# Performance work log

Measured on AMD Instinct MI355X. Metric: run time of the kernel, lower is better.

The kernel has to match this reference:

```python
import jax, jax.numpy as jnp
import numpy as np

B_LAYERS = 4      # no_of_base_layers
A = 2048          # no_of_aux_layers
E_LAYERS = 4      # no_of_end_layers
H = 256           # nodes_in_each_layer
IN = 1            # input_shape
OUT = 2           # output_shape
NUM_LAYERS = B_LAYERS + A + E_LAYERS + 1


def setup_inputs() -> dict:
    key = jax.random.key(0)
    ks = jax.random.split(key, 24)
    s = 0.02
    f32 = jnp.float32
    d = {}
    d["X"] = jax.random.normal(ks[0], (A,), f32)
    d["X_mask"] = jax.random.randint(ks[1], (A,), 0, 2) > 0
    d["base_feature"] = jax.random.normal(ks[2], (IN,), f32)
    # base stack: Linear(IN,H)+ReLU then (B_LAYERS-1) x Linear(H,H)+ReLU; per-layer out heads Linear(H,OUT)+Softmax
    d["Wb_first"] = jax.random.normal(ks[3], (IN, H), f32) * s
    d["bb_first"] = jnp.zeros((H,), f32)
    d["Wb_rest"] = jax.random.normal(ks[4], (B_LAYERS - 1, H, H), f32) * s
    d["bb_rest"] = jnp.zeros((B_LAYERS - 1, H), f32)
    d["Wbo"] = jax.random.normal(ks[5], (B_LAYERS, H, OUT), f32) * s
    d["bbo"] = jnp.zeros((B_LAYERS, OUT), f32)
    # middle layer
    d["Wm"] = jax.random.normal(ks[6], (H, H), f32) * s
    d["bm"] = jnp.zeros((H,), f32)
    d["Wmo"] = jax.random.normal(ks[7], (H, OUT), f32) * s
    d["bmo"] = jnp.zeros((OUT,), f32)
    # aux experts: A x (Linear(1,H)+ReLU) and A x (Linear(H,OUT)+Softmax)
    d["Wa"] = jax.random.normal(ks[8], (A, H), f32) * s
    d["ba"] = jnp.zeros((A, H), f32)
    d["Wao"] = jax.random.normal(ks[9], (A, H, OUT), f32) * s
    d["bao"] = jnp.zeros((A, OUT), f32)
    # end stack: Linear((A+1)*H, H) then (E_LAYERS-1) x Linear(H,H); per-layer heads
    d["We_first"] = jax.random.normal(ks[10], ((A + 1) * H, H), f32) * s
    d["be_first"] = jnp.zeros((H,), f32)
    d["We_rest"] = jax.random.normal(ks[11], (E_LAYERS - 1, H, H), f32) * s
    d["be_rest"] = jnp.zeros((E_LAYERS - 1, H), f32)
    d["Weo"] = jax.random.normal(ks[12], (E_LAYERS, H, OUT), f32) * s
    d["beo"] = jnp.zeros((E_LAYERS, OUT), f32)
    d["layer_weights"] = jnp.full((NUM_LAYERS,), 1.0 / NUM_LAYERS, f32)
    return d


def reference(X, X_mask, base_feature, Wb_first, bb_first, Wb_rest, bb_rest,
              Wbo, bbo, Wm, bm, Wmo, bmo, Wa, ba, Wao, bao,
              We_first, be_first, We_rest, be_rest, Weo, beo, layer_weights):
    dt = X.dtype
    # --- base stack ---
    x = base_feature.reshape(1, -1)
    x = jax.nn.relu(x @ Wb_first + bb_first)
    outs = [jax.nn.softmax(x @ Wbo[0] + bbo[0], axis=-1)]
    for i in range(B_LAYERS - 1):
        x = jax.nn.relu(x @ Wb_rest[i] + bb_rest[i])
        outs.append(jax.nn.softmax(x @ Wbo[i + 1] + bbo[i + 1], axis=-1))
    # --- middle ---
    middle = jax.nn.relu(x @ Wm + bm)                       # [1, H]
    middle_out = jax.nn.softmax(middle @ Wmo + bmo, axis=-1)
    # --- aux experts, vectorized over all A features (absent ones are masked out) ---
    h = jax.nn.relu(X[:, None] * Wa + ba)                   # [A, H]
    aux_out = jax.nn.softmax(jnp.einsum('ah,aho->ao', h, Wao) + bao, axis=-1)  # [A, OUT]
    mask = X_mask.astype(dt)                                # [A]
    # --- weighted scatter-combine into end_input ---
    end_input = jnp.concatenate([h * mask[:, None], middle], axis=0)  # [A+1, H]
    gamma = jnp.concatenate([layer_weights[B_LAYERS:B_LAYERS + A], layer_weights[-1:]])
    gmask = jnp.concatenate([mask, jnp.ones((1,), dt)])
    gamma = gamma * gmask
    gamma = gamma / jnp.sum(gamma)
    x = (end_input * gamma[:, None]).reshape(1, -1)         # [1, (A+1)*H]
    # --- end stack ---
    end_outs = []
    x = jax.nn.relu(x @ We_first + be_first)
    end_outs.append(jax.nn.softmax(x @ Weo[0] + beo[0], axis=-1))
    for i in range(E_LAYERS - 1):
        x = jax.nn.relu(x @ We_rest[i] + be_rest[i])
        end_outs.append(jax.nn.softmax(x @ Weo[i + 1] + beo[i + 1], axis=-1))
    # --- hedge-weighted combine (order: base, aux, end, middle == layer_weights order) ---
    logits = jnp.concatenate(outs + [aux_out] + end_outs + [middle_out], axis=0)  # [NUM_LAYERS, OUT]
    active = jnp.concatenate([jnp.ones((B_LAYERS,), dt), mask, jnp.ones((E_LAYERS + 1,), dt)])
    w = layer_weights * active
    w = w / jnp.sum(w)
    logits_w = logits * w[:, None]
    logit = jnp.sum(logits_w, axis=0)
    return (logit, logits_w)
```

## Files before the change

### kernel.cpp

```cpp
#include <hip/hip_runtime.h>
#include <math.h>

#define A_N 2048
#define NLAYERS 2057

#define PART_OFF  0
#define PART2_OFF 524544
#define GSUM_OFF  540928
#define WSUM_OFF  540929
#define NACTI_OFF 540930
#define LISTI_OFF 540932

typedef float f4 __attribute__((ext_vector_type(4)));

__device__ __forceinline__ void warmN(const float* base, int nf4, int t, int nthr)
{
    const f4* p = (const f4*)base;
    for (int i = t; i < nf4; i += nthr) {
        f4 v = p[i];
        asm volatile("" :: "v"(v.x), "v"(v.y), "v"(v.z), "v"(v.w));
    }
}


__device__ __forceinline__ void head256(const float* sx, float* r0, float* r1,
                                        const float* W2, const float* b2,
                                        float scale, float* dest, int t)
{
    float xv = sx[t];
    r0[t] = xv * W2[2*t];
    r1[t] = xv * W2[2*t+1];
    __syncthreads();
    for (int s = 128; s > 0; s >>= 1) {
        if (t < s) { r0[t] += r0[t+s]; r1[t] += r1[t+s]; }
        __syncthreads();
    }
    if (t == 0) {
        float o0 = r0[0] + b2[0], o1 = r1[0] + b2[1];
        float m  = fmaxf(o0, o1);
        float e0 = expf(o0 - m), e1 = expf(o1 - m);
        float inv = scale / (e0 + e1);
        dest[0] = e0 * inv;
        dest[1] = e1 * inv;
    }
    __syncthreads();
}

__device__ __forceinline__ int compact_nz(float val, int t, int quad, int lane,
                                          int* rlist, float* gl, int* swcnt)
{
    bool pred = (val != 0.f);
    unsigned long long m = __ballot(pred);
    if (lane == 0) swcnt[quad] = (int)__popcll(m);
    __syncthreads();
    int nr = swcnt[0] + swcnt[1] + swcnt[2] + swcnt[3];
    int offs = 0;
    #pragma unroll
    for (int q2 = 0; q2 < 4; ++q2) if (q2 < quad) offs += swcnt[q2];
    int rank = (int)__popcll(m & ((1ull << lane) - 1ull));
    if (pred) { rlist[offs + rank] = t; gl[offs + rank] = val; }
    if (t < 32) { rlist[nr + t] = 0; gl[nr + t] = 0.f; }
    __syncthreads();
    return nr;
}

__device__ __forceinline__ f4 gather8(const f4* Wb, const int* rlist,
                                      const float* gl, int nr, int quad)
{
    f4 acc = {0.f, 0.f, 0.f, 0.f};
    int niter = (nr + 31) >> 5;
    for (int it = 0; it < niter; ++it) {
        int base = it*32 + quad*8;
        int r0 = rlist[base+0], r1 = rlist[base+1], r2 = rlist[base+2], r3 = rlist[base+3];
        int r4 = rlist[base+4], r5 = rlist[base+5], r6 = rlist[base+6], r7 = rlist[base+7];
        float g0 = gl[base+0], g1 = gl[base+1], g2 = gl[base+2], g3 = gl[base+3];
        float g4 = gl[base+4], g5 = gl[base+5], g6 = gl[base+6], g7 = gl[base+7];
        f4 v0 = Wb[(size_t)r0*64]; f4 v1 = Wb[(size_t)r1*64];
        f4 v2 = Wb[(size_t)r2*64]; f4 v3 = Wb[(size_t)r3*64];
        f4 v4 = Wb[(size_t)r4*64]; f4 v5 = Wb[(size_t)r5*64];
        f4 v6 = Wb[(size_t)r6*64]; f4 v7 = Wb[(size_t)r7*64];
        acc += g0*v0 + g1*v1 + g2*v2 + g3*v3 + g4*v4 + g5*v5 + g6*v6 + g7*v7;
    }
    return acc;
}

__global__ __launch_bounds__(1024) void k_list(const int* __restrict__ Xm,
                                               const float* __restrict__ lw,
                                               const float* __restrict__ Wbr,
                                               const float* __restrict__ Wm,
                                               const float* __restrict__ Wbo,
                                               const float* __restrict__ Wmo,
                                               const float* __restrict__ Wef,
                                               float* __restrict__ out,
                                               float* __restrict__ ws)
{
    int t = threadIdx.x, b = blockIdx.x;
    if (b > 0) {
        int wi = b - 1;
        if      (wi < 12) warmN(Wbr + (size_t)wi * 16384, 4096, t, 1024);
        else if (wi < 16) warmN(Wm + (size_t)(wi - 12) * 16384, 4096, t, 1024);
        else if (wi == 16) { warmN(Wbo, 512, t, 1024); warmN(Wmo, 128, t, 1024); }
        else warmN(Wef + (size_t)A_N * 65536 + (size_t)(wi - 17) * 16384, 4096, t, 1024);
        return;
    }
    __shared__ int scan[1024];
    __shared__ float fred[1024];
    int e0 = 2*t, e1 = 2*t + 1;
    int a0 = (Xm[e0] != 0) ? 1 : 0;
    int a1 = (Xm[e1] != 0) ? 1 : 0;
    int s = a0 + a1;
    scan[t] = s;
    fred[t] = (a0 ? lw[4+e0] : 0.f) + (a1 ? lw[4+e1] : 0.f);
    __syncthreads();
    for (int off = 1; off < 1024; off <<= 1) {
        int v = (t >= off) ? scan[t-off] : 0;
        __syncthreads();
        scan[t] += v;
        __syncthreads();
    }
    for (int ss = 512; ss > 0; ss >>= 1) {
        if (t < ss) fred[t] += fred[t+ss];
        __syncthreads();
    }
    int total = scan[1023];
    int excl  = scan[t] - s;
    int* list = (int*)ws + LISTI_OFF;
    if (a0) list[excl] = e0;
    else    { out[2 + (4+e0)*2] = 0.f; out[2 + (4+e0)*2 + 1] = 0.f; }
    if (a1) list[excl + a0] = e1;
    else    { out[2 + (4+e1)*2] = 0.f; out[2 + (4+e1)*2 + 1] = 0.f; }
    if (t == 0) {
        ((int*)ws)[NACTI_OFF] = total;
        float gaux = fred[0];
        ws[GSUM_OFF] = gaux + lw[2056];
        ws[WSUM_OFF] = lw[0]+lw[1]+lw[2]+lw[3] + gaux
                     + lw[2052]+lw[2053]+lw[2054]+lw[2055]+lw[2056];
    }
}

__global__ __launch_bounds__(256, 4) void k_mainc(
    const float* __restrict__ X,
    const float* __restrict__ bfv,
    const float* __restrict__ Wbf, const float* __restrict__ bbf,
    const float* __restrict__ Wbr, const float* __restrict__ bbr,
    const float* __restrict__ Wbo, const float* __restrict__ bbo,
    const float* __restrict__ Wm, const float* __restrict__ bm,
    const float* __restrict__ Wmo, const float* __restrict__ bmo,
    const float* __restrict__ Wa, const float* __restrict__ ba,
    const float* __restrict__ Wao, const float* __restrict__ bao,
    const float* __restrict__ Wef, const float* __restrict__ lw,
    float* __restrict__ out, float* __restrict__ ws)
{
    __shared__ float sg[256];
    __shared__ float sacc[4][256];
    __shared__ float gl[288];
    __shared__ int   rlist[288];
    __shared__ int   swcnt[4];
    int b = blockIdx.x, t = threadIdx.x;
    int quad = t >> 6, lane = t & 63;
    float* part = ws + PART_OFF;

    if (b == 0) {
        sg[t] = fmaxf(bfv[0] * Wbf[t] + bbf[t], 0.f);
        __syncthreads();
        head256(sg, sacc[0], sacc[1], Wbo, bbo, lw[0], out + 2, t);

        #define MV_GATED(W, B)                                                  \
        {                                                                       \
            int nr = compact_nz(sg[t], t, quad, lane, rlist, gl, swcnt);        \
            f4 a = gather8((const f4*)(W) + lane, rlist, gl, nr, quad);         \
            sacc[quad][lane*4+0] = a.x; sacc[quad][lane*4+1] = a.y;             \
            sacc[quad][lane*4+2] = a.z; sacc[quad][lane*4+3] = a.w;             \
            __syncthreads();                                                    \
            float v = fmaxf(sacc[0][t] + sacc[1][t] + sacc[2][t] + sacc[3][t]   \
                            + (B)[t], 0.f);                                     \
            __syncthreads();                                                    \
            sg[t] = v;                                                          \
            __syncthreads();                                                    \
        }

        for (int i = 0; i < 3; ++i) {
            MV_GATED(Wbr + i*65536, bbr + i*256);
            head256(sg, sacc[0], sacc[1], Wbo + (i+1)*512, bbo + (i+1)*2,
                    lw[i+1], out + 2 + (i+1)*2, t);
        }
        MV_GATED(Wm, bm);
        head256(sg, sacc[0], sacc[1], Wmo, bmo, lw[2056], out + 2 + 2056*2, t);

        {
            int nr = compact_nz(sg[t] * lw[2056], t, quad, lane, rlist, gl, swcnt);
            f4 a = gather8((const f4*)(Wef + (size_t)A_N * 65536) + lane,
                           rlist, gl, nr, quad);
            sacc[quad][lane*4+0] = a.x; sacc[quad][lane*4+1] = a.y;
            sacc[quad][lane*4+2] = a.z; sacc[quad][lane*4+3] = a.w;
            __syncthreads();
            part[t] = sacc[0][t] + sacc[1][t] + sacc[2][t] + sacc[3][t];
        }
        return;
    }

    int idx = b - 1;
    int nact = ((const int*)ws)[NACTI_OFF];
    if (idx >= nact) return;
    int e = ((const int*)ws + LISTI_OFF)[idx];

    float xv = X[e];
    float w  = lw[4 + e];
    float h  = fmaxf(xv * Wa[e*256 + t] + ba[e*256 + t], 0.f);
    float2 wo = *(const float2*)&Wao[(size_t)e*512 + 2*t];
    sacc[0][t] = h * wo.x;
    sacc[1][t] = h * wo.y;
    __syncthreads();
    for (int s = 128; s > 0; s >>= 1) {
        if (t < s) { sacc[0][t] += sacc[0][t+s]; sacc[1][t] += sacc[1][t+s]; }
        __syncthreads();
    }
    if (t == 0) {
        float o0 = sacc[0][0] + bao[2*e], o1 = sacc[1][0] + bao[2*e+1];
        float m  = fmaxf(o0, o1);
        float e0 = expf(o0 - m), e1 = expf(o1 - m);
        float inv = w / (e0 + e1);
        out[2 + (4+e)*2]     = e0 * inv;
        out[2 + (4+e)*2 + 1] = e1 * inv;
    }
    float val = h * w;
    __syncthreads();

    int nr = compact_nz(val, t, quad, lane, rlist, gl, swcnt);
    f4 acc = gather8((const f4*)(Wef + (size_t)e * 65536) + lane, rlist, gl, nr, quad);
    sacc[quad][lane*4+0] = acc.x; sacc[quad][lane*4+1] = acc.y;
    sacc[quad][lane*4+2] = acc.z; sacc[quad][lane*4+3] = acc.w;
    __syncthreads();
    part[(size_t)(1+idx)*256 + t] = sacc[0][t] + sacc[1][t] + sacc[2][t] + sacc[3][t];
}

__global__ __launch_bounds__(256) void k_red(
    const float* __restrict__ Wer, const float* __restrict__ Weo,
    const float* __restrict__ bef, const float* __restrict__ ber,
    const float* __restrict__ beo, float* __restrict__ ws)
{
    int r = blockIdx.x, t = threadIdx.x;
    if (r < 48) warmN(Wer + (size_t)r * 4096, 1024, t, 256);
    else if (r == 48) {
        warmN(Weo, 512, t, 256); warmN(bef, 64, t, 256);
        warmN(ber, 192, t, 256); warmN(beo, 2, t, 256);
    }
    int nact = ((const int*)ws)[NACTI_OFF];
    float acc = 0.f;
    for (int j = r; j <= nact; j += 64) {
        acc += ws[PART_OFF + (size_t)j*256 + t];
    }
    ws[PART2_OFF + r*256 + t] = acc;
}

__global__ __launch_bounds__(1024) void k_end(
    const float* __restrict__ bef, const float* __restrict__ Wer,
    const float* __restrict__ ber, const float* __restrict__ Weo,
    const float* __restrict__ beo, const float* __restrict__ lw,
    float* __restrict__ out, float* __restrict__ ws)
{
    __shared__ float sx[256];
    __shared__ float racc[4][256];
    __shared__ float red0[1024], red1[1024];
    __shared__ float endraw[4][2];
    int tid = threadIdx.x;
    int q = tid >> 8, t = tid & 255;

    float acc = 0.f;
    #pragma unroll
    for (int j = 0; j < 16; ++j) acc += ws[PART2_OFF + (q*16 + j)*256 + t];
    racc[q][t] = acc;
    __syncthreads();
    float gsum = ws[GSUM_OFF];
    if (tid < 256) {
        float v = racc[0][t] + racc[1][t] + racc[2][t] + racc[3][t];
        sx[t] = fmaxf(v / gsum + bef[t], 0.f);
    }
    __syncthreads();

    #define HEAD_G(W2, B2, SCALE, DEST)                                         \
    {                                                                           \
        if (tid < 256) { red0[tid] = sx[tid]*(W2)[2*tid]; red1[tid] = sx[tid]*(W2)[2*tid+1]; } \
        __syncthreads();                                                        \
        for (int s = 128; s > 0; s >>= 1) {                                     \
            if (tid < s) { red0[tid] += red0[tid+s]; red1[tid] += red1[tid+s]; }\
            __syncthreads();                                                    \
        }                                                                       \
        if (tid == 0) {                                                         \
            float o0 = red0[0] + (B2)[0], o1 = red1[0] + (B2)[1];               \
            float m  = fmaxf(o0, o1);                                           \
            float e0 = expf(o0 - m), e1 = expf(o1 - m);                         \
            float inv = (SCALE) / (e0 + e1);                                    \
            (DEST)[0] = e0 * inv; (DEST)[1] = e1 * inv;                         \
        }                                                                       \
        __syncthreads();                                                        \
    }

    HEAD_G(Weo, beo, lw[2052], &endraw[0][0]);
    for (int i = 0; i < 3; ++i) {
        const float* Wq = Wer + i*65536 + (q*64)*256;
        float a2 = 0.f;
        #pragma unroll 16
        for (int k = 0; k < 64; ++k) a2 += sx[q*64 + k] * Wq[k*256 + t];
        racc[q][t] = a2;
        __syncthreads();
        if (tid < 256) {
            float v = racc[0][t] + racc[1][t] + racc[2][t] + racc[3][t];
            sx[t] = fmaxf(v + ber[i*256 + t], 0.f);
        }
        __syncthreads();
        HEAD_G(Weo + (i+1)*512, beo + (i+1)*2, lw[2053 + i], &endraw[i+1][0]);
    }

    float invw = 1.f / ws[WSUM_OFF];
    float s0 = 0.f, s1 = 0.f;
    for (int i = tid; i < NLAYERS; i += 1024) {
        float v0, v1;
        if (i >= 2052 && i < 2056) { v0 = endraw[i-2052][0]; v1 = endraw[i-2052][1]; }
        else                        { v0 = out[2 + 2*i];      v1 = out[2 + 2*i + 1]; }
        v0 *= invw; v1 *= invw;
        out[2 + 2*i]     = v0;
        out[2 + 2*i + 1] = v1;
        s0 += v0; s1 += v1;
    }
    red0[tid] = s0; red1[tid] = s1; __syncthreads();
    for (int s = 512; s > 0; s >>= 1) {
        if (tid < s) { red0[tid] += red0[tid+s]; red1[tid] += red1[tid+s]; }
        __syncthreads();
    }
    if (tid == 0) { out[0] = red0[0]; out[1] = red1[0]; }
}

extern "C" void kernel_launch(void* const* d_in, const int* in_sizes, int n_in,
                              void* d_out, int out_size, void* d_ws, size_t ws_size,
                              hipStream_t stream)
{
    const float* X    = (const float*)d_in[0];
    const int*   Xm   = (const int*)  d_in[1];
    const float* bfv  = (const float*)d_in[2];
    const float* Wbf  = (const float*)d_in[3];
    const float* bbf  = (const float*)d_in[4];
    const float* Wbr  = (const float*)d_in[5];
    const float* bbr  = (const float*)d_in[6];
    const float* Wbo  = (const float*)d_in[7];
    const float* bbo  = (const float*)d_in[8];
    const float* Wm   = (const float*)d_in[9];
    const float* bm   = (const float*)d_in[10];
    const float* Wmo  = (const float*)d_in[11];
    const float* bmo  = (const float*)d_in[12];
    const float* Wa   = (const float*)d_in[13];
    const float* ba   = (const float*)d_in[14];
    const float* Wao  = (const float*)d_in[15];
    const float* bao  = (const float*)d_in[16];
    const float* Wef  = (const float*)d_in[17];
    const float* bef  = (const float*)d_in[18];
    const float* Wer  = (const float*)d_in[19];
    const float* ber  = (const float*)d_in[20];
    const float* Weo  = (const float*)d_in[21];
    const float* beo  = (const float*)d_in[22];
    const float* lw   = (const float*)d_in[23];
    float* out = (float*)d_out;
    float* wsf = (float*)d_ws;

    k_list<<<22, 1024, 0, stream>>>(Xm, lw, Wbr, Wm, Wbo, Wmo, Wef, out, wsf);
    k_mainc<<<A_N + 1, 256, 0, stream>>>(X, bfv, Wbf, bbf, Wbr, bbr, Wbo, bbo,
                                         Wm, bm, Wmo, bmo, Wa, ba, Wao, bao,
                                         Wef, lw, out, wsf);
    k_red<<<64, 256, 0, stream>>>(Wer, Weo, bef, ber, beo, wsf);
    k_end<<<1, 1024, 0, stream>>>(bef, Wer, ber, Weo, beo, lw, out, wsf);
}
```

Baseline: 66.03 us.

## Drop the compaction kernel and gate aux blocks directly on the mask

Removes the k_list prefix-scan kernel, so each aux block now reads the mask and exits early when its expert is inactive. The cache-warming moves into the first blocks of the main kernel, and the gamma and weight sums are recomputed inside the final kernel. The end-stack matvec is also restructured to use 16 wavefronts with float4 loads. This saves one kernel launch and its serial scan, but k_red now walks all 2048 slots with a mask check, and the warming blocks delay aux expert work.

```diff
diff --git a/kernel.cpp b/kernel.cpp
--- a/kernel.cpp
+++ b/kernel.cpp
@@ -6,10 +6,6 @@
 
 #define PART_OFF  0
 #define PART2_OFF 524544
-#define GSUM_OFF  540928
-#define WSUM_OFF  540929
-#define NACTI_OFF 540930
-#define LISTI_OFF 540932
 
 typedef float f4 __attribute__((ext_vector_type(4)));
 
@@ -84,62 +80,8 @@
     return acc;
 }
 
-__global__ __launch_bounds__(1024) void k_list(const int* __restrict__ Xm,
-                                               const float* __restrict__ lw,
-                                               const float* __restrict__ Wbr,
-                                               const float* __restrict__ Wm,
-                                               const float* __restrict__ Wbo,
-                                               const float* __restrict__ Wmo,
-                                               const float* __restrict__ Wef,
-                                               float* __restrict__ out,
-                                               float* __restrict__ ws)
-{
-    int t = threadIdx.x, b = blockIdx.x;
-    if (b > 0) {
-        int wi = b - 1;
-        if      (wi < 12) warmN(Wbr + (size_t)wi * 16384, 4096, t, 1024);
-        else if (wi < 16) warmN(Wm + (size_t)(wi - 12) * 16384, 4096, t, 1024);
-        else if (wi == 16) { warmN(Wbo, 512, t, 1024); warmN(Wmo, 128, t, 1024); }
-        else warmN(Wef + (size_t)A_N * 65536 + (size_t)(wi - 17) * 16384, 4096, t, 1024);
-        return;
-    }
-    __shared__ int scan[1024];
-    __shared__ float fred[1024];
-    int e0 = 2*t, e1 = 2*t + 1;
-    int a0 = (Xm[e0] != 0) ? 1 : 0;
-    int a1 = (Xm[e1] != 0) ? 1 : 0;
-    int s = a0 + a1;
-    scan[t] = s;
-    fred[t] = (a0 ? lw[4+e0] : 0.f) + (a1 ? lw[4+e1] : 0.f);
-    __syncthreads();
-    for (int off = 1; off < 1024; off <<= 1) {
-        int v = (t >= off) ? scan[t-off] : 0;
-        __syncthreads();
-        scan[t] += v;
-        __syncthreads();
-    }
-    for (int ss = 512; ss > 0; ss >>= 1) {
-        if (t < ss) fred[t] += fred[t+ss];
-        __syncthreads();
-    }
-    int total = scan[1023];
-    int excl  = scan[t] - s;
-    int* list = (int*)ws + LISTI_OFF;
-    if (a0) list[excl] = e0;
-    else    { out[2 + (4+e0)*2] = 0.f; out[2 + (4+e0)*2 + 1] = 0.f; }
-    if (a1) list[excl + a0] = e1;
-    else    { out[2 + (4+e1)*2] = 0.f; out[2 + (4+e1)*2 + 1] = 0.f; }
-    if (t == 0) {
-        ((int*)ws)[NACTI_OFF] = total;
-        float gaux = fred[0];
-        ws[GSUM_OFF] = gaux + lw[2056];
-        ws[WSUM_OFF] = lw[0]+lw[1]+lw[2]+lw[3] + gaux
-                     + lw[2052]+lw[2053]+lw[2054]+lw[2055]+lw[2056];
-    }
-}
-
 __global__ __launch_bounds__(256, 4) void k_mainc(
-    const float* __restrict__ X,
+    const float* __restrict__ X, const int* __restrict__ Xm,
     const float* __restrict__ bfv,
     const float* __restrict__ Wbf, const float* __restrict__ bbf,
     const float* __restrict__ Wbr, const float* __restrict__ bbr,
@@ -199,10 +141,20 @@
         return;
     }
 
-    int idx = b - 1;
-    int nact = ((const int*)ws)[NACTI_OFF];
-    if (idx >= nact) return;
-    int e = ((const int*)ws + LISTI_OFF)[idx];
+    int e = b - 1;
+
+    if (b <= 21) {
+        int wi = b - 1;
+        if      (wi < 12) warmN(Wbr + (size_t)wi * 16384, 4096, t, 256);
+        else if (wi < 16) warmN(Wm + (size_t)(wi - 12) * 16384, 4096, t, 256);
+        else if (wi == 16) { warmN(Wbo, 512, t, 256); warmN(Wmo, 128, t, 256); }
+        else warmN(Wef + (size_t)A_N * 65536 + (size_t)(wi - 17) * 16384, 4096, t, 256);
+    }
+
+    if (Xm[e] == 0) {
+        if (t == 0) { out[2 + (4+e)*2] = 0.f; out[2 + (4+e)*2 + 1] = 0.f; }
+        return;
+    }
 
     float xv = X[e];
     float w  = lw[4 + e];
@@ -231,10 +183,11 @@
     sacc[quad][lane*4+0] = acc.x; sacc[quad][lane*4+1] = acc.y;
     sacc[quad][lane*4+2] = acc.z; sacc[quad][lane*4+3] = acc.w;
     __syncthreads();
-    part[(size_t)(1+idx)*256 + t] = sacc[0][t] + sacc[1][t] + sacc[2][t] + sacc[3][t];
+    part[(size_t)(1+e)*256 + t] = sacc[0][t] + sacc[1][t] + sacc[2][t] + sacc[3][t];
 }
 
 __global__ __launch_bounds__(256) void k_red(
+    const int* __restrict__ Xm,
     const float* __restrict__ Wer, const float* __restrict__ Weo,
     const float* __restrict__ bef, const float* __restrict__ ber,
     const float* __restrict__ beo, float* __restrict__ ws)
@@ -245,38 +198,61 @@
         warmN(Weo, 512, t, 256); warmN(bef, 64, t, 256);
         warmN(ber, 192, t, 256); warmN(beo, 2, t, 256);
     }
-    int nact = ((const int*)ws)[NACTI_OFF];
     float acc = 0.f;
-    for (int j = r; j <= nact; j += 64) {
-        acc += ws[PART_OFF + (size_t)j*256 + t];
+    for (int j = r; j <= A_N; j += 64) {
+        if (j == 0 || Xm[j-1] != 0) acc += ws[PART_OFF + (size_t)j*256 + t];
     }
     ws[PART2_OFF + r*256 + t] = acc;
 }
 
 __global__ __launch_bounds__(1024) void k_end(
+    const int* __restrict__ Xm,
     const float* __restrict__ bef, const float* __restrict__ Wer,
     const float* __restrict__ ber, const float* __restrict__ Weo,
     const float* __restrict__ beo, const float* __restrict__ lw,
     float* __restrict__ out, float* __restrict__ ws)
 {
     __shared__ float sx[256];
-    __shared__ float racc[4][256];
+    __shared__ float wacc[16][256];
     __shared__ float red0[1024], red1[1024];
     __shared__ float endraw[4][2];
+    __shared__ float sgsum, swsum;
     int tid = threadIdx.x;
+    int w = tid >> 6, l = tid & 63;
     int q = tid >> 8, t = tid & 255;
 
-    float acc = 0.f;
-    #pragma unroll
-    for (int j = 0; j < 16; ++j) acc += ws[PART2_OFF + (q*16 + j)*256 + t];
-    racc[q][t] = acc;
-    __syncthreads();
-    float gsum = ws[GSUM_OFF];
-    if (tid < 256) {
-        float v = racc[0][t] + racc[1][t] + racc[2][t] + racc[3][t];
-        sx[t] = fmaxf(v / gsum + bef[t], 0.f);
-    }
-    __syncthreads();
+    {
+        int ea = 2*tid, eb = 2*tid + 1;
+        float g = 0.f;
+        if (Xm[ea] != 0) g += lw[4 + ea];
+        if (Xm[eb] != 0) g += lw[4 + eb];
+        red0[tid] = g;
+        __syncthreads();
+        for (int s = 512; s > 0; s >>= 1) {
+            if (tid < s) red0[tid] += red0[tid+s];
+            __syncthreads();
+        }
+        if (tid == 0) {
+            float gaux = red0[0];
+            sgsum = gaux + lw[2056];
+            swsum = lw[0]+lw[1]+lw[2]+lw[3] + gaux
+                  + lw[2052]+lw[2053]+lw[2054]+lw[2055]+lw[2056];
+        }
+        __syncthreads();
+    }
+
+    {
+        float acc = 0.f;
+        #pragma unroll
+        for (int j = 0; j < 16; ++j) acc += ws[PART2_OFF + ((tid>>8)*16 + j)*256 + t];
+        wacc[q][t] = acc;
+        __syncthreads();
+        if (tid < 256) {
+            float v = wacc[0][t] + wacc[1][t] + wacc[2][t] + wacc[3][t];
+            sx[t] = fmaxf(v / sgsum + bef[t], 0.f);
+        }
+        __syncthreads();
+    }
 
     #define HEAD_G(W2, B2, SCALE, DEST)                                         \
     {                                                                           \
@@ -296,23 +272,36 @@
         __syncthreads();                                                        \
     }
 
+    #define MV_E(W, B)                                                          \
+    {                                                                           \
+        const f4* Wv = (const f4*)(W);                                          \
+        f4 a4 = {0.f, 0.f, 0.f, 0.f};                                           \
+        _Pragma("unroll 16")                                                    \
+        for (int kk = 0; kk < 16; ++kk) {                                       \
+            int k = w*16 + kk;                                                  \
+            float xv = sx[k];                                                   \
+            f4 wv = Wv[k*64 + l];                                               \
+            a4 += xv * wv;                                                      \
+        }                                                                       \
+        wacc[w][4*l+0] = a4.x; wacc[w][4*l+1] = a4.y;                           \
+        wacc[w][4*l+2] = a4.z; wacc[w][4*l+3] = a4.w;                           \
+        __syncthreads();                                                        \
+        if (tid < 256) {                                                        \
+            float v = 0.f;                                                      \
+            _Pragma("unroll 16")                                                \
+            for (int j = 0; j < 16; ++j) v += wacc[j][tid];                     \
+            sx[tid] = fmaxf(v + (B)[tid], 0.f);                                 \
+        }                                                                       \
+        __syncthreads();                                                        \
+    }
+
     HEAD_G(Weo, beo, lw[2052], &endraw[0][0]);
     for (int i = 0; i < 3; ++i) {
-        const float* Wq = Wer + i*65536 + (q*64)*256;
-        float a2 = 0.f;
-        #pragma unroll 16
-        for (int k = 0; k < 64; ++k) a2 += sx[q*64 + k] * Wq[k*256 + t];
-        racc[q][t] = a2;
-        __syncthreads();
-        if (tid < 256) {
-            float v = racc[0][t] + racc[1][t] + racc[2][t] + racc[3][t];
-            sx[t] = fmaxf(v + ber[i*256 + t], 0.f);
-        }
-        __syncthreads();
+        MV_E(Wer + i*65536, ber + i*256);
         HEAD_G(Weo + (i+1)*512, beo + (i+1)*2, lw[2053 + i], &endraw[i+1][0]);
     }
 
-    float invw = 1.f / ws[WSUM_OFF];
+    float invw = 1.f / swsum;
     float s0 = 0.f, s1 = 0.f;
     for (int i = tid; i < NLAYERS; i += 1024) {
         float v0, v1;
@@ -362,10 +351,9 @@
     float* out = (float*)d_out;
     float* wsf = (float*)d_ws;
 
-    k_list<<<22, 1024, 0, stream>>>(Xm, lw, Wbr, Wm, Wbo, Wmo, Wef, out, wsf);
-    k_mainc<<<A_N + 1, 256, 0, stream>>>(X, bfv, Wbf, bbf, Wbr, bbr, Wbo, bbo,
+    k_mainc<<<A_N + 1, 256, 0, stream>>>(X, Xm, bfv, Wbf, bbf, Wbr, bbr, Wbo, bbo,
                                          Wm, bm, Wmo, bmo, Wa, ba, Wao, bao,
                                          Wef, lw, out, wsf);
-    k_red<<<64, 256, 0, stream>>>(Wer, Weo, bef, ber, beo, wsf);
-    k_end<<<1, 1024, 0, stream>>>(bef, Wer, ber, Weo, beo, lw, out, wsf);
-}
+    k_red<<<64, 256, 0, stream>>>(Xm, Wer, Weo, bef, ber, beo, wsf);
+    k_end<<<1, 1024, 0, stream>>>(Xm, bef, Wer, ber, Weo, beo, lw, out, wsf);
+}
```

Result: slower. 70.48 us (+6.7%).
